# Performance work log

Measured on AMD Instinct MI355X. Metric: run time of the kernel, lower is better.

## Reference

```python
import jax, jax.numpy as jnp
import numpy as np

D = 384        # model dim
H = 6          # heads
HD = 64        # head dim (inner_dim = H*HD = 384)
DEPTH = 12
P = 16         # patch size
G = 14         # grid side (224/16)
NP = G * G     # 196 patches
NC = 1000
B = 64
DFF = 4 * D
SCALE = HD ** -0.5
EPS = 1e-5


def _ln(x, w, b):
    m = x.mean(-1, keepdims=True)
    v = ((x - m) ** 2).mean(-1, keepdims=True)
    return (x - m) * jax.lax.rsqrt(v + EPS) * w + b


def setup_inputs() -> dict:
    key = jax.random.key(0)
    ks = jax.random.split(key, 16)
    s = 0.02
    inp = {
        "x": jax.random.normal(ks[0], (B, 3, 224, 224), jnp.float32),
        # patch embedding conv as matmul: weight [3*P*P, D]
        "W_patch": jax.random.normal(ks[1], (3 * P * P, D), jnp.float32) * s,
        "b_patch": jnp.zeros((D,), jnp.float32),
        "ln0_w": jnp.ones((D,), jnp.float32),
        "ln0_b": jnp.zeros((D,), jnp.float32),
        "pos_emb": jax.random.normal(ks[2], (1, NP + 1, D), jnp.float32) * s,
        "cls_token": jax.random.normal(ks[3], (1, D), jnp.float32),
        # per-block params stacked over depth
        "ln1_w": jnp.ones((DEPTH, D), jnp.float32),
        "ln1_b": jnp.zeros((DEPTH, D), jnp.float32),
        "Wq": jax.random.normal(ks[4], (DEPTH, D, H * HD), jnp.float32) * s,
        "Wkv": jax.random.normal(ks[5], (DEPTH, D, 2 * H * HD), jnp.float32) * s,
        "Wo": jax.random.normal(ks[6], (DEPTH, H * HD, D), jnp.float32) * s,
        "bo": jnp.zeros((DEPTH, D), jnp.float32),
        "ln2_w": jnp.ones((DEPTH, D), jnp.float32),
        "ln2_b": jnp.zeros((DEPTH, D), jnp.float32),
        "W1": jax.random.normal(ks[7], (DEPTH, D, DFF), jnp.float32) * s,
        "b1": jnp.zeros((DEPTH, DFF), jnp.float32),
        "W2": jax.random.normal(ks[8], (DEPTH, DFF, D), jnp.float32) * s,
        "b2": jnp.zeros((DEPTH, D), jnp.float32),
        "lnf_w": jnp.ones((D,), jnp.float32),
        "lnf_b": jnp.zeros((D,), jnp.float32),
        "Whead": jax.random.normal(ks[9], (D, NC), jnp.float32) * s,
        "bhead": jnp.zeros((NC,), jnp.float32),
    }
    return inp


def reference(x, W_patch, b_patch, ln0_w, ln0_b, pos_emb, cls_token,
              ln1_w, ln1_b, Wq, Wkv, Wo, bo, ln2_w, ln2_b,
              W1, b1, W2, b2, lnf_w, lnf_b, Whead, bhead):
    b = x.shape[0]
    # patch embed: Conv2d(3, D, P, stride=P) == extract patches + matmul
    patches = x.reshape(b, 3, G, P, G, P).transpose(0, 2, 4, 1, 3, 5).reshape(b, NP, 3 * P * P)
    h = patches @ W_patch + b_patch                     # [b, NP, D]
    h = _ln(h, ln0_w, ln0_b)
    cls = jnp.broadcast_to(cls_token[None], (b, 1, D))
    h = jnp.concatenate([cls, h], axis=1) + pos_emb     # [b, NP+1, D]
    n = NP + 1
    for d in range(DEPTH):
        # self-attention with pre-LN, residual
        a = _ln(h, ln1_w[d], ln1_b[d])
        q = (a @ Wq[d]).reshape(b, n, H, HD).transpose(0, 2, 1, 3)
        kv = a @ Wkv[d]
        k = kv[..., : H * HD].reshape(b, n, H, HD).transpose(0, 2, 1, 3)
        v = kv[..., H * HD:].reshape(b, n, H, HD).transpose(0, 2, 1, 3)
        sim = jnp.einsum('bhid,bhjd->bhij', q, k) * SCALE
        attn = jax.nn.softmax(sim, axis=-1)
        o = jnp.einsum('bhij,bhjd->bhid', attn, v)
        o = o.transpose(0, 2, 1, 3).reshape(b, n, H * HD)
        h = h + o @ Wo[d] + bo[d]
        # MLP with pre-LN, residual, exact GELU
        m = _ln(h, ln2_w[d], ln2_b[d])
        m = jax.nn.gelu(m @ W1[d] + b1[d], approximate=False)
        h = h + m @ W2[d] + b2[d]
    cls_out = h[:, 0, :]
    logits = _ln(cls_out, lnf_w, lnf_b) @ Whead + bhead
    return logits
```

## Files before the change

### kernel.cpp

```cpp
#include <hip/hip_runtime.h>


typedef unsigned short u16;
typedef __attribute__((ext_vector_type(8))) short short8;
typedef __attribute__((ext_vector_type(4))) float f32x4;
typedef __attribute__((ext_vector_type(4))) unsigned short u16x4;
typedef __attribute__((ext_vector_type(2))) unsigned short u16x2;

#define D_      384
#define NH      6
#define DEPTH_  12
#define NP_     196
#define NT_     197
#define B_      64
#define DFF_    1536
#define M_REAL  (B_*NT_)
#define M_PAD   12672
#define M_PATCH (B_*NP_)

__device__ __forceinline__ float bf2f(u16 u){
  unsigned int i = ((unsigned int)u) << 16;
  return __builtin_bit_cast(float, i);
}
__device__ __forceinline__ u16 f2bf(float f){
  unsigned int i = __builtin_bit_cast(unsigned int, f);
  i = (i + 0x7FFFu + ((i >> 16) & 1u)) >> 16;
  return (u16)i;
}
__device__ __forceinline__ float gelu_f(float x){
  float t = x * (1.595769122f + 0.0713548162726f * x * x);
  return x / (1.f + __expf(-t));
}

#define GLOAD_LDS16(g, l) __builtin_amdgcn_global_load_lds( \
    (const __attribute__((address_space(1))) void*)(g),      \
    (__attribute__((address_space(3))) void*)(l), 16, 0, 0)

#define MFMA_BF16(a, b, c) __builtin_amdgcn_mfma_f32_16x16x32_bf16((a), (b), (c), 0, 0, 0)

__global__ __launch_bounds__(256) void transpose_cvt(const float* __restrict__ src,
                                                     u16* __restrict__ dst, int K, int N,
                                                     int Nsrc,
                                                     size_t sstride, size_t dstride)
{
  __shared__ float tile[32][33];
  src += blockIdx.z * sstride;
  dst += blockIdx.z * dstride;
  int tx = threadIdx.x, ty = threadIdx.y;
  int n0 = blockIdx.x * 32, k0 = blockIdx.y * 32;
#pragma unroll
  for (int i = 0; i < 4; ++i){
    float v = 0.f;
    if (n0 + tx < Nsrc) v = src[(size_t)(k0 + ty + i*8) * Nsrc + n0 + tx];
    tile[ty + i*8][tx] = v;
  }
  __syncthreads();
#pragma unroll
  for (int i = 0; i < 4; ++i)
    dst[(size_t)(n0 + ty + i*8) * K + k0 + tx] = f2bf(tile[tx][ty + i*8]);
}

__global__ __launch_bounds__(256) void patch_extract(const float* __restrict__ x,
                                                     u16* __restrict__ patches)
{
  int r = blockIdx.x;
  int b = r / NP_, p = r % NP_;
  int gy = p / 14, gx = p % 14;
  int t = threadIdx.x;
  int py = t >> 4, px = t & 15;
#pragma unroll
  for (int c = 0; c < 3; ++c){
    float v = x[(((size_t)b*3 + c)*224 + gy*16 + py)*224 + gx*16 + px];
    patches[(size_t)r*768 + c*256 + t] = f2bf(v);
  }
}

template<int MODE, int BM, int BN, int KS>
__global__ __launch_bounds__(256) void gemm_k(const u16* __restrict__ A,
                                              const u16* __restrict__ Bt,
                                              const float* __restrict__ bias,
                                              u16* __restrict__ outb,
                                              float* __restrict__ outf,
                                              int N, int K, int nbx, size_t sstride)
{
  constexpr int MI = BM/32;
  constexpr int NJ = BN/32;
  constexpr int L  = BM/64 + BN/64;
  constexpr int WM = BM/2, WN = BN/2;
  __shared__ u16 lds[2*(BM+BN)*32];
  u16* As = lds;
  u16* Bs = lds + 2*BM*32;
  int tid = threadIdx.x;
  int w = tid >> 6, lane = tid & 63;

  int nwg = gridDim.x;
  int q = nwg >> 3, r = nwg & 7;
  int xcd = blockIdx.x & 7, slot = blockIdx.x >> 3;
  int wgid = (xcd < r ? xcd*(q+1) : r*(q+1) + (xcd - r)*q) + slot;
  int m0 = (wgid / nbx) * BM;
  int n0 = (wgid % nbx) * BN;
  int kz = (KS > 1) ? blockIdx.y : 0;
  int Kl = K / KS;
  int koff = kz * Kl;
  int wr = w >> 1, wc = w & 1;

  f32x4 acc[MI][NJ];
#pragma unroll
  for (int i = 0; i < MI; ++i)
#pragma unroll
    for (int j = 0; j < NJ; ++j) acc[i][j] = (f32x4){0.f,0.f,0.f,0.f};

  int srow = lane >> 2;
  int skc  = ((lane & 3) ^ (srow & 3)) * 8;
  const u16* Ag = A  + (size_t)(m0 + w*16 + srow) * K + koff + skc;
  const u16* Bg = Bt + (size_t)(n0 + w*16 + srow) * K + koff + skc;

  int fr  = lane & 15;
  int fsw = ((lane >> 4) ^ (lane & 3)) << 3;

  auto stage = [&](int bi, int kt){
    u16* Ad = As + bi*(BM*32) + (w*16)*32;
    u16* Bd = Bs + bi*(BN*32) + (w*16)*32;
#pragma unroll
    for (int c = 0; c < BM/64; ++c)
      GLOAD_LDS16(Ag + (size_t)(c*64)*K + kt, Ad + c*64*32);
#pragma unroll
    for (int c = 0; c < BN/64; ++c)
      GLOAD_LDS16(Bg + (size_t)(c*64)*K + kt, Bd + c*64*32);
  };
  auto compute = [&](int bi){
    const u16* Ab = As + bi*(BM*32);
    const u16* Bb = Bs + bi*(BN*32);
    short8 af[MI], bfr[NJ];
#pragma unroll
    for (int i = 0; i < MI; ++i)
      af[i]  = *(const short8*)&Ab[(wr*WM + i*16 + fr)*32 + fsw];
#pragma unroll
    for (int j = 0; j < NJ; ++j)
      bfr[j] = *(const short8*)&Bb[(wc*WN + j*16 + fr)*32 + fsw];
#pragma unroll
    for (int i = 0; i < MI; ++i)
#pragma unroll
      for (int j = 0; j < NJ; ++j)
        acc[i][j] = MFMA_BF16(af[i], bfr[j], acc[i][j]);
  };

  int nk = Kl >> 5;
  stage(0, 0);
  for (int t = 0; t < nk; ++t){
    int b = t & 1;
    if (t + 1 < nk) stage(b ^ 1, (t + 1) * 32);
    __builtin_amdgcn_sched_barrier(0);
    if (t + 1 < nk){
      if constexpr (L == 2)      asm volatile("s_waitcnt vmcnt(2)" ::: "memory");
      else if constexpr (L == 3) asm volatile("s_waitcnt vmcnt(3)" ::: "memory");
      else                       asm volatile("s_waitcnt vmcnt(4)" ::: "memory");
    } else {
      asm volatile("s_waitcnt vmcnt(0)" ::: "memory");
    }
    __builtin_amdgcn_s_barrier();
    asm volatile("" ::: "memory");
    compute(b);
    __builtin_amdgcn_sched_barrier(0);
    __builtin_amdgcn_s_barrier();
  }

  int cr = (lane >> 4) << 2;
  int cc = lane & 15;

  if constexpr (MODE == 3){
#pragma unroll
    for (int j = 0; j < NJ; ++j){
      int c = n0 + wc*WN + j*16 + cc;
      float bv = bias ? bias[c] : 0.f;
#pragma unroll
      for (int i = 0; i < MI; ++i){
        int rbase = m0 + wr*WM + i*16 + cr;
#pragma unroll
        for (int e = 0; e < 4; ++e){
          float v = acc[i][j][e] + bv;
          if (c < N) outf[(size_t)(rbase + e) * N + c] = v;
        }
      }
    }
  } else {
    constexpr int PITCH = WN + 8;
    u16* Cs = lds + w * (16 * PITCH);
    u16* outp = (MODE == 4) ? outb + (size_t)kz * sstride : outb;
    int lr0 = lane >> 3;
    int lc  = lane & 7;
#pragma unroll
    for (int i = 0; i < MI; ++i){
#pragma unroll
      for (int j = 0; j < NJ; ++j){
        int c = n0 + wc*WN + j*16 + cc;
        float bv = (bias && kz == 0) ? bias[c] : 0.f;
#pragma unroll
        for (int e = 0; e < 4; ++e){
          float v = acc[i][j][e] + bv;
          if (MODE == 2) v = gelu_f(v);
          Cs[(cr + e) * PITCH + j*16 + cc] = f2bf(v);
        }
      }
#pragma unroll
      for (int p = 0; p < 2; ++p){
        int lr = p*8 + lr0;
        short8 val = *(const short8*)&Cs[lr * PITCH + lc*8];
        size_t gm = (size_t)(m0 + wr*WM + i*16 + lr);
        *(short8*)&outp[gm * N + n0 + wc*WN + lc*8] = val;
      }
    }
  }
}

__global__ __launch_bounds__(256) void ln_rows(const float* __restrict__ in,
                                               const float* __restrict__ gw,
                                               const float* __restrict__ gb,
                                               u16* __restrict__ out, int rows,
                                               size_t rstride)
{
  int m = blockIdx.x * 4 + (threadIdx.x >> 6);
  int lane = threadIdx.x & 63;
  if (m >= rows) return;
  const float* r = in + (size_t)m * rstride;
  float4 v0 = *(const float4*)(r + lane*4);
  float2 v1 = *(const float2*)(r + 256 + lane*2);
  float sum = v0.x+v0.y+v0.z+v0.w+v1.x+v1.y;
  float sq  = v0.x*v0.x+v0.y*v0.y+v0.z*v0.z+v0.w*v0.w+v1.x*v1.x+v1.y*v1.y;
#pragma unroll
  for (int d = 1; d < 64; d <<= 1){ sum += __shfl_xor(sum, d); sq += __shfl_xor(sq, d); }
  float mean = sum * (1.f/D_);
  float rs = rsqrtf(sq*(1.f/D_) - mean*mean + 1e-5f);
  float4 w0 = *(const float4*)(gw + lane*4);
  float2 w1 = *(const float2*)(gw + 256 + lane*2);
  float4 b0 = *(const float4*)(gb + lane*4);
  float2 b1v= *(const float2*)(gb + 256 + lane*2);
  u16x4 o4 = { f2bf((v0.x-mean)*rs*w0.x + b0.x), f2bf((v0.y-mean)*rs*w0.y + b0.y),
               f2bf((v0.z-mean)*rs*w0.z + b0.z), f2bf((v0.w-mean)*rs*w0.w + b0.w) };
  u16x2 o2 = { f2bf((v1.x-mean)*rs*w1.x + b1v.x), f2bf((v1.y-mean)*rs*w1.y + b1v.y) };
  *(u16x4*)(out + (size_t)m*D_ + lane*4) = o4;
  *(u16x2*)(out + (size_t)m*D_ + 256 + lane*2) = o2;
}

__global__ __launch_bounds__(256) void ln_rows_add(const float* __restrict__ in,
                                                   const u16* __restrict__ s0,
                                                   const u16* __restrict__ s1,
                                                   const float* __restrict__ gw,
                                                   const float* __restrict__ gb,
                                                   u16* __restrict__ out,
                                                   float* __restrict__ hout,
                                                   int rows, size_t rstride)
{
  int m = blockIdx.x * 4 + (threadIdx.x >> 6);
  int lane = threadIdx.x & 63;
  if (m >= rows) return;
  const float* r = in + (size_t)m * rstride;
  const u16* p0 = s0 + (size_t)m * rstride;
  const u16* p1 = s1 + (size_t)m * rstride;
  float4 v0 = *(const float4*)(r + lane*4);
  float2 v1 = *(const float2*)(r + 256 + lane*2);
  u16x4 a0 = *(const u16x4*)(p0 + lane*4);
  u16x2 a1 = *(const u16x2*)(p0 + 256 + lane*2);
  u16x4 c0 = *(const u16x4*)(p1 + lane*4);
  u16x2 c1 = *(const u16x2*)(p1 + 256 + lane*2);
  float x0 = v0.x + bf2f(a0.x) + bf2f(c0.x);
  float x1 = v0.y + bf2f(a0.y) + bf2f(c0.y);
  float x2 = v0.z + bf2f(a0.z) + bf2f(c0.z);
  float x3 = v0.w + bf2f(a0.w) + bf2f(c0.w);
  float x4 = v1.x + bf2f(a1.x) + bf2f(c1.x);
  float x5 = v1.y + bf2f(a1.y) + bf2f(c1.y);
  float sum = x0+x1+x2+x3+x4+x5;
  float sq  = x0*x0+x1*x1+x2*x2+x3*x3+x4*x4+x5*x5;
#pragma unroll
  for (int d = 1; d < 64; d <<= 1){ sum += __shfl_xor(sum, d); sq += __shfl_xor(sq, d); }
  float mean = sum * (1.f/D_);
  float rs = rsqrtf(sq*(1.f/D_) - mean*mean + 1e-5f);
  float4 w0 = *(const float4*)(gw + lane*4);
  float2 w1 = *(const float2*)(gw + 256 + lane*2);
  float4 b0 = *(const float4*)(gb + lane*4);
  float2 b1v= *(const float2*)(gb + 256 + lane*2);
  u16x4 o4 = { f2bf((x0-mean)*rs*w0.x + b0.x), f2bf((x1-mean)*rs*w0.y + b0.y),
               f2bf((x2-mean)*rs*w0.z + b0.z), f2bf((x3-mean)*rs*w0.w + b0.w) };
  u16x2 o2 = { f2bf((x4-mean)*rs*w1.x + b1v.x), f2bf((x5-mean)*rs*w1.y + b1v.y) };
  *(u16x4*)(out + (size_t)m*D_ + lane*4) = o4;
  *(u16x2*)(out + (size_t)m*D_ + 256 + lane*2) = o2;
  if (hout){
    float* ho = hout + (size_t)m * rstride;
    float4 h0 = {x0,x1,x2,x3};
    float2 h1 = {x4,x5};
    *(float4*)(ho + lane*4) = h0;
    *(float2*)(ho + 256 + lane*2) = h1;
  }
}

__global__ __launch_bounds__(256) void assemble_h(const u16* __restrict__ pe,
                                                  const float* __restrict__ gw,
                                                  const float* __restrict__ gb,
                                                  const float* __restrict__ pos,
                                                  const float* __restrict__ cls,
                                                  float* __restrict__ h)
{
  int m = blockIdx.x * 4 + (threadIdx.x >> 6);
  int lane = threadIdx.x & 63;
  if (m >= M_PAD) return;
  float* ho = h + (size_t)m * D_;
  if (m >= M_REAL){
    float4 z = {0.f,0.f,0.f,0.f};
    *(float4*)(ho + lane*4) = z;
    float2 z2 = {0.f,0.f};
    *(float2*)(ho + 256 + lane*2) = z2;
    return;
  }
  int b = m / NT_, t = m % NT_;
  const float* pr = pos + (size_t)t * D_;
  float4 p0 = *(const float4*)(pr + lane*4);
  float2 p1 = *(const float2*)(pr + 256 + lane*2);
  if (t == 0){
    float4 c0 = *(const float4*)(cls + lane*4);
    float2 c1 = *(const float2*)(cls + 256 + lane*2);
    float4 r0 = {c0.x+p0.x, c0.y+p0.y, c0.z+p0.z, c0.w+p0.w};
    float2 r1 = {c1.x+p1.x, c1.y+p1.y};
    *(float4*)(ho + lane*4) = r0;
    *(float2*)(ho + 256 + lane*2) = r1;
  } else {
    const u16* per = pe + (size_t)(b*NP_ + (t-1)) * D_;
    u16x4 a0 = *(const u16x4*)(per + lane*4);
    u16x2 a1 = *(const u16x2*)(per + 256 + lane*2);
    float x0=bf2f(a0.x), x1=bf2f(a0.y), x2=bf2f(a0.z), x3=bf2f(a0.w), x4=bf2f(a1.x), x5=bf2f(a1.y);
    float sum = x0+x1+x2+x3+x4+x5;
    float sq  = x0*x0+x1*x1+x2*x2+x3*x3+x4*x4+x5*x5;
#pragma unroll
    for (int d = 1; d < 64; d <<= 1){ sum += __shfl_xor(sum, d); sq += __shfl_xor(sq, d); }
    float mean = sum * (1.f/D_);
    float rs = rsqrtf(sq*(1.f/D_) - mean*mean + 1e-5f);
    float4 w0 = *(const float4*)(gw + lane*4);
    float2 w1 = *(const float2*)(gw + 256 + lane*2);
    float4 b0 = *(const float4*)(gb + lane*4);
    float2 b1v= *(const float2*)(gb + 256 + lane*2);
    float4 r0 = { (x0-mean)*rs*w0.x + b0.x + p0.x, (x1-mean)*rs*w0.y + b0.y + p0.y,
                  (x2-mean)*rs*w0.z + b0.z + p0.z, (x3-mean)*rs*w0.w + b0.w + p0.w };
    float2 r1 = { (x4-mean)*rs*w1.x + b1v.x + p1.x, (x5-mean)*rs*w1.y + b1v.y + p1.y };
    *(float4*)(ho + lane*4) = r0;
    *(float2*)(ho + 256 + lane*2) = r1;
  }
}

__global__ __launch_bounds__(256) void attn_k(const u16* __restrict__ qkv,
                                              u16* __restrict__ o)
{
  __shared__ u16 Ks[208*72];
  __shared__ u16 Vt[64*232];
  __shared__ u16 Ps[4][16*40];
  int bh = blockIdx.x;
  int b = bh / NH, hh = bh % NH;
  int tid = threadIdx.x, w = tid >> 6, lane = tid & 63;
  const u16* kbase = qkv + (size_t)b*NT_*1152 + 384 + hh*64;
  const u16* vbase = kbase + 384;

  int jr = tid >> 3, col = (tid & 7) * 8;
#pragma unroll
  for (int it = 0; it < 7; ++it){
    int j = it*32 + jr;
    if (j < 208){
      uint4 val = {0u,0u,0u,0u};
      if (j < 197) val = *(const uint4*)(kbase + (size_t)j*1152 + col);
      *(uint4*)&Ks[j*72 + col] = val;
    }
  }
#pragma unroll
  for (int it = 0; it < 7; ++it){
    int j = it*32 + jr;
    union { uint4 v; u16 s[8]; } u;
    u.v.x = 0u; u.v.y = 0u; u.v.z = 0u; u.v.w = 0u;
    if (j < 197) u.v = *(const uint4*)(vbase + (size_t)j*1152 + col);
#pragma unroll
    for (int e = 0; e < 8; ++e) Vt[(size_t)(col+e)*232 + j] = u.s[e];
  }
  __syncthreads();

  u16* myP = Ps[w];
  int fr = lane & 15, fk = lane >> 4;

  for (int qt = w; qt < 13; qt += 4){
    const u16* qrow = qkv + (size_t)(b*NT_ + qt*16 + fr)*1152 + hh*64 + fk*8;
    short8 aq0 = *(const short8*)qrow;
    short8 aq1 = *(const short8*)(qrow + 32);

    f32x4 s[13];
#pragma unroll
    for (int jt = 0; jt < 13; ++jt){
      const u16* kr = &Ks[(jt*16 + fr)*72 + fk*8];
      short8 bk0 = *(const short8*)kr;
      short8 bk1 = *(const short8*)(kr + 32);
      f32x4 z = {0.f,0.f,0.f,0.f};
      z = MFMA_BF16(aq0, bk0, z);
      z = MFMA_BF16(aq1, bk1, z);
      s[jt] = z;
    }

#pragma unroll
    for (int e = 0; e < 4; ++e){
      float mx = -1e30f;
#pragma unroll
      for (int jt = 0; jt < 13; ++jt){
        int cj = jt*16 + fr;
        float v = (cj < NT_) ? s[jt][e]*0.125f : -1e30f;
        s[jt][e] = v;
        mx = fmaxf(mx, v);
      }
#pragma unroll
      for (int d = 1; d < 16; d <<= 1) mx = fmaxf(mx, __shfl_xor(mx, d));
      float su = 0.f;
#pragma unroll
      for (int jt = 0; jt < 13; ++jt){
        float p = __expf(s[jt][e] - mx);
        s[jt][e] = p; su += p;
      }
#pragma unroll
      for (int d = 1; d < 16; d <<= 1) su += __shfl_xor(su, d);
      float ri = 1.f / su;
#pragma unroll
      for (int jt = 0; jt < 13; ++jt) s[jt][e] *= ri;
    }

    f32x4 oacc[4];
#pragma unroll
    for (int dt = 0; dt < 4; ++dt) oacc[dt] = (f32x4){0.f,0.f,0.f,0.f};
#pragma unroll
    for (int jc = 0; jc < 7; ++jc){
#pragma unroll
      for (int jtl = 0; jtl < 2; ++jtl){
        int jt = jc*2 + jtl;
#pragma unroll
        for (int e = 0; e < 4; ++e){
          u16 pv = 0;
          if (jt < 13) pv = f2bf(s[jt][e]);
          myP[(fk*4 + e)*40 + jtl*16 + fr] = pv;
        }
      }
      asm volatile("s_waitcnt lgkmcnt(0)" ::: "memory");
      short8 pa = *(const short8*)&myP[fr*40 + fk*8];
#pragma unroll
      for (int dt = 0; dt < 4; ++dt){
        short8 bv = *(const short8*)&Vt[(size_t)(dt*16 + fr)*232 + jc*32 + fk*8];
        oacc[dt] = MFMA_BF16(pa, bv, oacc[dt]);
      }
    }

#pragma unroll
    for (int dt = 0; dt < 4; ++dt)
#pragma unroll
      for (int e = 0; e < 4; ++e){
        int t = qt*16 + fk*4 + e;
        if (t < NT_)
          o[(size_t)(b*NT_ + t)*384 + hh*64 + dt*16 + fr] = f2bf(oacc[dt][e]);
      }
  }
}

extern "C" void kernel_launch(void* const* d_in, const int* in_sizes, int n_in,
                              void* d_out, int out_size, void* d_ws, size_t ws_size,
                              hipStream_t stream)
{
  (void)in_sizes; (void)n_in; (void)out_size; (void)ws_size;
  const float* x_in    = (const float*)d_in[0];
  const float* W_patch = (const float*)d_in[1];
  const float* b_patch = (const float*)d_in[2];
  const float* ln0_w   = (const float*)d_in[3];
  const float* ln0_b   = (const float*)d_in[4];
  const float* pos_emb = (const float*)d_in[5];
  const float* cls_tok = (const float*)d_in[6];
  const float* ln1_w   = (const float*)d_in[7];
  const float* ln1_b   = (const float*)d_in[8];
  const float* Wq      = (const float*)d_in[9];
  const float* Wkv     = (const float*)d_in[10];
  const float* Wo      = (const float*)d_in[11];
  const float* bo      = (const float*)d_in[12];
  const float* ln2_w   = (const float*)d_in[13];
  const float* ln2_b   = (const float*)d_in[14];
  const float* W1      = (const float*)d_in[15];
  const float* b1      = (const float*)d_in[16];
  const float* W2      = (const float*)d_in[17];
  const float* b2      = (const float*)d_in[18];
  const float* lnf_w   = (const float*)d_in[19];
  const float* lnf_b   = (const float*)d_in[20];
  const float* Whead   = (const float*)d_in[21];
  const float* bhead   = (const float*)d_in[22];

  char* ws = (char*)d_ws;
  size_t off = 0;
  auto nxt = [&](size_t bytes)->char* {
    char* p = ws + off;
    off += (bytes + 255) & ~(size_t)255;
    return p;
  };
  u16*   g_buf   = (u16*)  nxt((size_t)M_PAD * DFF_ * 2);
  float* hbuf    = (float*)nxt((size_t)M_PAD * D_ * 4);
  u16*   abuf    = (u16*)  nxt((size_t)M_PAD * D_ * 2);
  u16*   qkvbuf  = (u16*)  nxt((size_t)M_PAD * 1152 * 2);
  u16*   obuf    = (u16*)  nxt((size_t)M_PAD * D_ * 2);
  u16*   sbuf    = (u16*)  nxt((size_t)2 * M_PAD * D_ * 2);
  u16*   lncls   = (u16*)  nxt((size_t)B_ * D_ * 2);
  u16*   whT     = (u16*)  nxt((size_t)1024 * D_ * 2);
  u16*   wT      = (u16*)  nxt((size_t)21528576 * 2);

  const size_t SS = (size_t)M_PAD * D_;
  u16* patches = g_buf;
  u16* pebuf   = abuf;
  u16* wpT   = wT;
  u16* wqkvT = wpT   + 294912;
  u16* woT   = wqkvT + 12*442368;
  u16* w1T   = woT   + 12*147456;
  u16* w2T   = w1T   + 12*589824;

  dim3 tpb(32, 8);
  transpose_cvt<<<dim3(12, 24, 1),  tpb, 0, stream>>>(W_patch, wpT, 768, 384, 384, 0, 0);
  transpose_cvt<<<dim3(12, 12, 12), tpb, 0, stream>>>(Wq,  wqkvT,            384, 384, 384,
                                                      (size_t)384*384, (size_t)1152*384);
  transpose_cvt<<<dim3(24, 12, 12), tpb, 0, stream>>>(Wkv, wqkvT + 384*384,  384, 768, 768,
                                                      (size_t)384*768, (size_t)1152*384);
  transpose_cvt<<<dim3(12, 12, 12), tpb, 0, stream>>>(Wo,  woT, 384, 384, 384,
                                                      (size_t)384*384, (size_t)384*384);
  transpose_cvt<<<dim3(48, 12, 12), tpb, 0, stream>>>(W1,  w1T, 384, 1536, 1536,
                                                      (size_t)384*1536, (size_t)384*1536);
  transpose_cvt<<<dim3(12, 48, 12), tpb, 0, stream>>>(W2,  w2T, 1536, 384, 384,
                                                      (size_t)1536*384, (size_t)1536*384);
  transpose_cvt<<<dim3(32, 12, 1),  tpb, 0, stream>>>(Whead, whT, 384, 1024, 1000, 0, 0);

  patch_extract<<<M_PATCH, 256, 0, stream>>>(x_in, patches);
  gemm_k<0,64,128,1><<<3*(M_PATCH/64), 256, 0, stream>>>(patches, wpT, b_patch, pebuf, nullptr, 384, 768, 3, 0);
  assemble_h<<<M_PAD/4, 256, 0, stream>>>(pebuf, ln0_w, ln0_b, pos_emb, cls_tok, hbuf);

  for (int d = 0; d < DEPTH_; ++d){
    if (d == 0)
      ln_rows<<<M_PAD/4, 256, 0, stream>>>(hbuf, ln1_w, ln1_b, abuf, M_PAD, D_);
    else
      ln_rows_add<<<M_PAD/4, 256, 0, stream>>>(hbuf, sbuf, sbuf + SS,
                                               ln1_w + d*384, ln1_b + d*384,
                                               abuf, hbuf, M_PAD, D_);
    gemm_k<0,128,128,1><<<9*(M_PAD/128), 256, 0, stream>>>(abuf, wqkvT + (size_t)d*442368, nullptr, qkvbuf, nullptr, 1152, 384, 9, 0);
    attn_k<<<B_*NH, 256, 0, stream>>>(qkvbuf, obuf);
    gemm_k<4,128,128,2><<<dim3(3*(M_PAD/128), 2), 256, 0, stream>>>(obuf, woT + (size_t)d*147456, bo + d*384, sbuf, nullptr, 384, 384, 3, SS);
    ln_rows_add<<<M_PAD/4, 256, 0, stream>>>(hbuf, sbuf, sbuf + SS,
                                             ln2_w + d*384, ln2_b + d*384,
                                             abuf, hbuf, M_PAD, D_);
    gemm_k<2,128,128,1><<<12*(M_PAD/128), 256, 0, stream>>>(abuf, w1T + (size_t)d*589824, b1 + d*1536, g_buf, nullptr, 1536, 384, 12, 0);
    gemm_k<4,128,128,2><<<dim3(3*(M_PAD/128), 2), 256, 0, stream>>>(g_buf, w2T + (size_t)d*589824, b2 + d*384, sbuf, nullptr, 384, 1536, 3, SS);
  }

  ln_rows_add<<<B_/4, 256, 0, stream>>>(hbuf, sbuf, sbuf + SS,
                                        lnf_w, lnf_b, lncls, nullptr,
                                        B_, (size_t)NT_*D_);
  gemm_k<3,64,64,1><<<16, 256, 0, stream>>>(lncls, whT, bhead, nullptr, (float*)d_out, 1000, 384, 16, 0);
}
```

Before: 1.854 ms.

## Use 8-wave GEMM workgroups, unroll K loop by two, merge weight transposes

The GEMM kernel gets a wave-count template parameter. All large GEMMs now launch 512-thread workgroups of 8 waves, each computing a 32x64 sub-tile of the 128x128 tile, and the patch-embedding GEMM grows from 64x128 to 128x128 tiles. The double-buffered K loop is unrolled by two so buffer indices are compile-time constants. The seven weight transpose/convert launches are folded into one kernel driven by a job table. The aim is more waves per CU to hide latency and fewer launches, at the cost of less register-level reuse per wave and an assumption that the K-step count is even.

```diff
diff --git a/kernel.cpp b/kernel.cpp
--- a/kernel.cpp
+++ b/kernel.cpp
@@ -38,16 +38,29 @@
 
 #define MFMA_BF16(a, b, c) __builtin_amdgcn_mfma_f32_16x16x32_bf16((a), (b), (c), 0, 0, 0)
 
-__global__ __launch_bounds__(256) void transpose_cvt(const float* __restrict__ src,
-                                                     u16* __restrict__ dst, int K, int N,
-                                                     int Nsrc,
-                                                     size_t sstride, size_t dstride)
+struct TJobs {
+  const float* src[7];
+  u16*         dst[7];
+  int          N[7], K[7], Nsrc[7];
+  long long    ss[7], ds[7];
+  int          cnt[7];
+};
+
+__global__ __launch_bounds__(256) void transpose_all(TJobs J)
 {
   __shared__ float tile[32][33];
-  src += blockIdx.z * sstride;
-  dst += blockIdx.z * dstride;
+  int local = blockIdx.x;
+  int j = 0;
+  while (local >= J.cnt[j]) { local -= J.cnt[j]; ++j; }
+  int nbx = J.N[j] >> 5, nby = J.K[j] >> 5;
+  int z   = local / (nbx * nby);
+  int rem = local - z * nbx * nby;
+  int by = rem / nbx, bx = rem - by * nbx;
+  const float* src = J.src[j] + (long long)z * J.ss[j];
+  u16* dst = J.dst[j] + (long long)z * J.ds[j];
+  int K = J.K[j], Nsrc = J.Nsrc[j];
   int tx = threadIdx.x, ty = threadIdx.y;
-  int n0 = blockIdx.x * 32, k0 = blockIdx.y * 32;
+  int n0 = bx * 32, k0 = by * 32;
 #pragma unroll
   for (int i = 0; i < 4; ++i){
     float v = 0.f;
@@ -75,18 +88,22 @@
   }
 }
 
-template<int MODE, int BM, int BN, int KS>
-__global__ __launch_bounds__(256) void gemm_k(const u16* __restrict__ A,
-                                              const u16* __restrict__ Bt,
-                                              const float* __restrict__ bias,
-                                              u16* __restrict__ outb,
-                                              float* __restrict__ outf,
-                                              int N, int K, int nbx, size_t sstride)
-{
-  constexpr int MI = BM/32;
-  constexpr int NJ = BN/32;
-  constexpr int L  = BM/64 + BN/64;
-  constexpr int WM = BM/2, WN = BN/2;
+template<int MODE, int BM, int BN, int KS, int NW>
+__global__ __launch_bounds__(NW*64) void gemm_k(const u16* __restrict__ A,
+                                                const u16* __restrict__ Bt,
+                                                const float* __restrict__ bias,
+                                                u16* __restrict__ outb,
+                                                float* __restrict__ outf,
+                                                int N, int K, int nbx, size_t sstride)
+{
+  constexpr int WAVES_M = (NW == 8) ? 4 : 2;
+  constexpr int WM = BM / WAVES_M;
+  constexpr int WN = BN / 2;
+  constexpr int MI = WM / 16;
+  constexpr int NJ = WN / 16;
+  constexpr int CA = BM / (16 * NW);
+  constexpr int CB = BN / (16 * NW);
+  constexpr int L  = CA + CB;
   __shared__ u16 lds[2*(BM+BN)*32];
   u16* As = lds;
   u16* Bs = lds + 2*BM*32;
@@ -122,11 +139,11 @@
     u16* Ad = As + bi*(BM*32) + (w*16)*32;
     u16* Bd = Bs + bi*(BN*32) + (w*16)*32;
 #pragma unroll
-    for (int c = 0; c < BM/64; ++c)
-      GLOAD_LDS16(Ag + (size_t)(c*64)*K + kt, Ad + c*64*32);
-#pragma unroll
-    for (int c = 0; c < BN/64; ++c)
-      GLOAD_LDS16(Bg + (size_t)(c*64)*K + kt, Bd + c*64*32);
+    for (int c = 0; c < CA; ++c)
+      GLOAD_LDS16(Ag + (size_t)(c*16*NW)*K + kt, Ad + c*16*NW*32);
+#pragma unroll
+    for (int c = 0; c < CB; ++c)
+      GLOAD_LDS16(Bg + (size_t)(c*16*NW)*K + kt, Bd + c*16*NW*32);
   };
   auto compute = [&](int bi){
     const u16* Ab = As + bi*(BM*32);
@@ -145,25 +162,38 @@
         acc[i][j] = MFMA_BF16(af[i], bfr[j], acc[i][j]);
   };
 
+#define WAIT_L()  do { \
+    if constexpr (L == 2)      asm volatile("s_waitcnt vmcnt(2)" ::: "memory"); \
+    else if constexpr (L == 3) asm volatile("s_waitcnt vmcnt(3)" ::: "memory"); \
+    else                       asm volatile("s_waitcnt vmcnt(4)" ::: "memory"); \
+  } while (0)
+
   int nk = Kl >> 5;
   stage(0, 0);
-  for (int t = 0; t < nk; ++t){
-    int b = t & 1;
-    if (t + 1 < nk) stage(b ^ 1, (t + 1) * 32);
+  for (int t = 0; t < nk; t += 2){
+    stage(1, (t + 1) * 32);
     __builtin_amdgcn_sched_barrier(0);
-    if (t + 1 < nk){
-      if constexpr (L == 2)      asm volatile("s_waitcnt vmcnt(2)" ::: "memory");
-      else if constexpr (L == 3) asm volatile("s_waitcnt vmcnt(3)" ::: "memory");
-      else                       asm volatile("s_waitcnt vmcnt(4)" ::: "memory");
-    } else {
-      asm volatile("s_waitcnt vmcnt(0)" ::: "memory");
-    }
+    WAIT_L();
     __builtin_amdgcn_s_barrier();
     asm volatile("" ::: "memory");
-    compute(b);
+    compute(0);
     __builtin_amdgcn_sched_barrier(0);
     __builtin_amdgcn_s_barrier();
-  }
+    if (t + 2 < nk){
+      stage(0, (t + 2) * 32);
+      __builtin_amdgcn_sched_barrier(0);
+      WAIT_L();
+    } else {
+      __builtin_amdgcn_sched_barrier(0);
+      asm volatile("s_waitcnt vmcnt(0)" ::: "memory");
+    }
+    __builtin_amdgcn_s_barrier();
+    asm volatile("" ::: "memory");
+    compute(1);
+    __builtin_amdgcn_sched_barrier(0);
+    __builtin_amdgcn_s_barrier();
+  }
+#undef WAIT_L
 
   int cr = (lane >> 4) << 2;
   int cc = lane & 15;
@@ -513,22 +543,25 @@
   u16* w1T   = woT   + 12*147456;
   u16* w2T   = w1T   + 12*589824;
 
-  dim3 tpb(32, 8);
-  transpose_cvt<<<dim3(12, 24, 1),  tpb, 0, stream>>>(W_patch, wpT, 768, 384, 384, 0, 0);
-  transpose_cvt<<<dim3(12, 12, 12), tpb, 0, stream>>>(Wq,  wqkvT,            384, 384, 384,
-                                                      (size_t)384*384, (size_t)1152*384);
-  transpose_cvt<<<dim3(24, 12, 12), tpb, 0, stream>>>(Wkv, wqkvT + 384*384,  384, 768, 768,
-                                                      (size_t)384*768, (size_t)1152*384);
-  transpose_cvt<<<dim3(12, 12, 12), tpb, 0, stream>>>(Wo,  woT, 384, 384, 384,
-                                                      (size_t)384*384, (size_t)384*384);
-  transpose_cvt<<<dim3(48, 12, 12), tpb, 0, stream>>>(W1,  w1T, 384, 1536, 1536,
-                                                      (size_t)384*1536, (size_t)384*1536);
-  transpose_cvt<<<dim3(12, 48, 12), tpb, 0, stream>>>(W2,  w2T, 1536, 384, 384,
-                                                      (size_t)1536*384, (size_t)1536*384);
-  transpose_cvt<<<dim3(32, 12, 1),  tpb, 0, stream>>>(Whead, whT, 384, 1024, 1000, 0, 0);
+  TJobs J;
+  auto setj = [&](int i, const float* s, u16* d, int N, int K, int Nsrc,
+                  long long ss, long long ds, int nz){
+    J.src[i]=s; J.dst[i]=d; J.N[i]=N; J.K[i]=K; J.Nsrc[i]=Nsrc;
+    J.ss[i]=ss; J.ds[i]=ds; J.cnt[i]=(N/32)*(K/32)*nz;
+  };
+  setj(0, W_patch, wpT,             384,  768,  384, 0, 0, 1);
+  setj(1, Wq,      wqkvT,           384,  384,  384, 384LL*384,  1152LL*384, 12);
+  setj(2, Wkv,     wqkvT + 384*384, 768,  384,  768, 384LL*768,  1152LL*384, 12);
+  setj(3, Wo,      woT,             384,  384,  384, 384LL*384,  384LL*384,  12);
+  setj(4, W1,      w1T,             1536, 384, 1536, 384LL*1536, 384LL*1536, 12);
+  setj(5, W2,      w2T,             384, 1536,  384, 1536LL*384, 1536LL*384, 12);
+  setj(6, Whead,   whT,             1024, 384, 1000, 0, 0, 1);
+  int tblocks = 0;
+  for (int i = 0; i < 7; ++i) tblocks += J.cnt[i];
+  transpose_all<<<tblocks, dim3(32,8), 0, stream>>>(J);
 
   patch_extract<<<M_PATCH, 256, 0, stream>>>(x_in, patches);
-  gemm_k<0,64,128,1><<<3*(M_PATCH/64), 256, 0, stream>>>(patches, wpT, b_patch, pebuf, nullptr, 384, 768, 3, 0);
+  gemm_k<0,128,128,1,8><<<3*(M_PATCH/128), 512, 0, stream>>>(patches, wpT, b_patch, pebuf, nullptr, 384, 768, 3, 0);
   assemble_h<<<M_PAD/4, 256, 0, stream>>>(pebuf, ln0_w, ln0_b, pos_emb, cls_tok, hbuf);
 
   for (int d = 0; d < DEPTH_; ++d){
@@ -538,18 +571,18 @@
       ln_rows_add<<<M_PAD/4, 256, 0, stream>>>(hbuf, sbuf, sbuf + SS,
                                                ln1_w + d*384, ln1_b + d*384,
                                                abuf, hbuf, M_PAD, D_);
-    gemm_k<0,128,128,1><<<9*(M_PAD/128), 256, 0, stream>>>(abuf, wqkvT + (size_t)d*442368, nullptr, qkvbuf, nullptr, 1152, 384, 9, 0);
+    gemm_k<0,128,128,1,8><<<9*(M_PAD/128), 512, 0, stream>>>(abuf, wqkvT + (size_t)d*442368, nullptr, qkvbuf, nullptr, 1152, 384, 9, 0);
     attn_k<<<B_*NH, 256, 0, stream>>>(qkvbuf, obuf);
-    gemm_k<4,128,128,2><<<dim3(3*(M_PAD/128), 2), 256, 0, stream>>>(obuf, woT + (size_t)d*147456, bo + d*384, sbuf, nullptr, 384, 384, 3, SS);
+    gemm_k<4,128,128,2,8><<<dim3(3*(M_PAD/128), 2), 512, 0, stream>>>(obuf, woT + (size_t)d*147456, bo + d*384, sbuf, nullptr, 384, 384, 3, SS);
     ln_rows_add<<<M_PAD/4, 256, 0, stream>>>(hbuf, sbuf, sbuf + SS,
                                              ln2_w + d*384, ln2_b + d*384,
                                              abuf, hbuf, M_PAD, D_);
-    gemm_k<2,128,128,1><<<12*(M_PAD/128), 256, 0, stream>>>(abuf, w1T + (size_t)d*589824, b1 + d*1536, g_buf, nullptr, 1536, 384, 12, 0);
-    gemm_k<4,128,128,2><<<dim3(3*(M_PAD/128), 2), 256, 0, stream>>>(g_buf, w2T + (size_t)d*589824, b2 + d*384, sbuf, nullptr, 384, 1536, 3, SS);
+    gemm_k<2,128,128,1,8><<<12*(M_PAD/128), 512, 0, stream>>>(abuf, w1T + (size_t)d*589824, b1 + d*1536, g_buf, nullptr, 1536, 384, 12, 0);
+    gemm_k<4,128,128,2,8><<<dim3(3*(M_PAD/128), 2), 512, 0, stream>>>(g_buf, w2T + (size_t)d*589824, b2 + d*384, sbuf, nullptr, 384, 1536, 3, SS);
   }
 
   ln_rows_add<<<B_/4, 256, 0, stream>>>(hbuf, sbuf, sbuf + SS,
                                         lnf_w, lnf_b, lncls, nullptr,
                                         B_, (size_t)NT_*D_);
-  gemm_k<3,64,64,1><<<16, 256, 0, stream>>>(lncls, whT, bhead, nullptr, (float*)d_out, 1000, 384, 16, 0);
-}
+  gemm_k<3,64,64,1,4><<<16, 256, 0, stream>>>(lncls, whT, bhead, nullptr, (float*)d_out, 1000, 384, 16, 0);
+}
```

New measurement: 1.804 ms. 2.7% less time.
